# Performance work log

Measured on AMD Instinct MI355X. Metric: run time of the kernel, lower is better.

Reference implementation:

```python
import jax, jax.numpy as jnp
import numpy as np

N_NODES, N_EDGES, D, H = 100000, 640000, 128, 128


def setup_inputs() -> dict:
    key = jax.random.key(0)
    k = jax.random.split(key, 5)
    x = jax.random.normal(k[0], (N_NODES, D), dtype=jnp.float32)
    edge_idx = jax.random.randint(k[1], (2, N_EDGES), 0, N_NODES)
    eps = jnp.zeros((1,), dtype=jnp.float32)  # nn.Parameter(torch.zeros(1))
    # MLP params: Linear(D,H) -> ReLU -> Linear(H,D)
    W1 = jax.random.normal(k[2], (D, H), dtype=jnp.float32) / np.sqrt(D).astype(np.float32)
    b1 = jnp.zeros((H,), dtype=jnp.float32)
    W2 = jax.random.normal(k[3], (H, D), dtype=jnp.float32) / np.sqrt(H).astype(np.float32)
    b2 = jnp.zeros((D,), dtype=jnp.float32)
    return dict(x=x, edge_idx=edge_idx, eps=eps, W1=W1, b1=b1, W2=W2, b2=b2)


def reference(x, edge_idx, eps, W1, b1, W2, b2):
    # gather src node features, scatter-add into dst rows
    src, dst = edge_idx[0], edge_idx[1]
    agg = jax.ops.segment_sum(x[src], dst, num_segments=x.shape[0])  # [N, D]
    out = (1.0 + eps) * x + agg  # eps-weighted residual
    h = jax.nn.relu(out @ W1 + b1)
    return h @ W2 + b2
```

## Files before the change

### kernel.cpp

```cpp
#include <hip/hip_runtime.h>

#define DD 128
typedef unsigned int uint;
typedef unsigned short ushort;

typedef __attribute__((ext_vector_type(8))) __bf16 bf16x8;
typedef __attribute__((ext_vector_type(8))) short short8;
typedef __attribute__((ext_vector_type(4))) float f32x4;

__device__ inline short f2bf_bits(float f) {
  union { float f; unsigned u; } x; x.f = f;
  unsigned r = x.u + 0x7fffu + ((x.u >> 16) & 1u);
  return (short)(r >> 16);
}
__device__ inline float bflo(uint u) { return __uint_as_float(u << 16); }
__device__ inline float bfhi(uint u) { return __uint_as_float(u & 0xffff0000u); }

__global__ void k_zero(int* __restrict__ p, int n) {
  int i = blockIdx.x * blockDim.x + threadIdx.x;
  if (i < n) p[i] = 0;
}

#define CHUNK 2048
__global__ __launch_bounds__(256) void k_bin(const int* __restrict__ ei, int ne,
                                             int* __restrict__ scur, uint* __restrict__ pairs32,
                                             const float4* __restrict__ xf4,
                                             short8* __restrict__ xb8, int nx8,
                                             const float* __restrict__ W1,
                                             const float* __restrict__ W2,
                                             ushort* __restrict__ wbf, int nbins) {
  __shared__ uint st[CHUNK];
  __shared__ ushort stb[CHUNK];
  __shared__ int hist[512];
  __shared__ int sc[512];
  __shared__ int loff[512];
  __shared__ int cur[512];
  __shared__ int gb[512];

  const int tid = threadIdx.x;
  const int sb = blockIdx.x & 63;
  const long base = (long)blockIdx.x * CHUNK;
  int m = (int)(ne - base);
  if (m > CHUNK) m = CHUNK;
  if (m < 0) m = 0;

  const int i0 = tid, i1 = tid + 256;
  hist[i0] = 0; hist[i1] = 0;
  cur[i0] = 0;  cur[i1] = 0;
  __syncthreads();

  uint wreg[8];
  int breg[8];
#pragma unroll
  for (int i = 0; i < 8; ++i) {
    int idx = i * 256 + tid;
    if (idx < m) {
      uint s = (uint)ei[base + idx];
      uint d = (uint)ei[(long)ne + base + idx];
      breg[i] = (int)(d >> 8);
      wreg[i] = (s << 8) | (d & 255u);
      atomicAdd(&hist[breg[i]], 1);
    } else {
      breg[i] = -1;
    }
  }
  __syncthreads();

  sc[i0] = hist[i0]; sc[i1] = hist[i1];
  __syncthreads();
  for (int d = 1; d < 512; d <<= 1) {
    int t0 = (i0 >= d) ? sc[i0 - d] : 0;
    int t1 = (i1 >= d) ? sc[i1 - d] : 0;
    __syncthreads();
    sc[i0] += t0; sc[i1] += t1;
    __syncthreads();
  }
  loff[i0] = sc[i0] - hist[i0];
  loff[i1] = sc[i1] - hist[i1];
  if (i0 < nbins && hist[i0] > 0) gb[i0] = atomicAdd(&scur[i0 * 64 + sb], hist[i0]);
  if (i1 < nbins && hist[i1] > 0) gb[i1] = atomicAdd(&scur[i1 * 64 + sb], hist[i1]);
  __syncthreads();

#pragma unroll
  for (int i = 0; i < 8; ++i) {
    if (breg[i] >= 0) {
      int p = atomicAdd(&cur[breg[i]], 1);
      int pos = loff[breg[i]] + p;
      st[pos] = wreg[i];
      stb[pos] = (ushort)breg[i];
    }
  }
  __syncthreads();

  for (int i = tid; i < m; i += 256) {
    int b = stb[i];
    int k = i - loff[b];
    int g = gb[b] + k;
    if (g < 128)
      pairs32[(long)b * 16384 + (sb << 8) + g] = st[i];
  }

  int t = blockIdx.x * 256 + tid;
  int stride = gridDim.x * 256;
  for (int c = t; c < nx8; c += stride) {
    float4 a = xf4[2 * c], b = xf4[2 * c + 1];
    short8 o;
    o[0] = f2bf_bits(a.x); o[1] = f2bf_bits(a.y); o[2] = f2bf_bits(a.z); o[3] = f2bf_bits(a.w);
    o[4] = f2bf_bits(b.x); o[5] = f2bf_bits(b.y); o[6] = f2bf_bits(b.z); o[7] = f2bf_bits(b.w);
    xb8[c] = o;
  }
  if (t < 16384) {
    int k = t >> 7, n = t & 127;
    wbf[128 * n + 8 * ((k >> 3) ^ (n & 7)) + (k & 7)] = (ushort)f2bf_bits(W1[t]);
  } else if (t < 32768) {
    int e = t - 16384;
    int k = e >> 7, n = e & 127;
    wbf[16384 + 128 * n + 8 * ((k >> 3) ^ (n & 7)) + (k & 7)] = (ushort)f2bf_bits(W2[e]);
  }
}

#define SUBCAP 128
__global__ __launch_bounds__(256) void k_bucket(const uint* __restrict__ pairs32,
                                                const int* __restrict__ scur,
                                                int* __restrict__ slot,
                                                int* __restrict__ cnt, int n) {
  __shared__ uint st[64 * SUBCAP];
  __shared__ int cs[64];
  __shared__ int cur[256];
  const int b = blockIdx.x;
  const int tid = threadIdx.x;
  if (tid < 64) {
    int c = scur[b * 64 + tid];
    cs[tid] = c < SUBCAP ? c : SUBCAP;
  }
  cur[tid] = 0;
  __syncthreads();
  for (int k = tid; k < 64 * SUBCAP; k += 256) {
    int s = k >> 7, i = k & (SUBCAP - 1);
    if (i < cs[s]) st[k] = pairs32[(long)b * 16384 + (s << 8) + i];
  }
  __syncthreads();
  for (int k = tid; k < 64 * SUBCAP; k += 256) {
    int s = k >> 7, i = k & (SUBCAP - 1);
    if (i < cs[s]) {
      uint w = st[k];
      int d = (int)(w & 255u);
      int p = atomicAdd(&cur[d], 1);
      if (p < 64) slot[(long)b * 16384 + d * 64 + p] = (int)(w >> 8);
    }
  }
  __syncthreads();
  int node = (b << 8) + tid;
  if (node < n) cnt[node] = cur[tid];
}

__global__ __launch_bounds__(256) void k_agg4(const uint* __restrict__ xb,
                                              const float* __restrict__ eps,
                                              const int* __restrict__ cnt,
                                              const int* __restrict__ slot,
                                              uint* __restrict__ agb, int n) {
  int wv = (blockIdx.x * 256 + threadIdx.x) >> 6;
  int lane = threadIdx.x & 63;
  int r0 = wv * 4;
  if (r0 >= n) return;
  float s = 1.0f + eps[0];

  float ax[4], ay[4];
  int m[4], src[4];
  int mm = 0;
#pragma unroll
  for (int q = 0; q < 4; ++q) {
    int r = r0 + q;
    if (r < n) {
      uint u = xb[(long)r * 64 + lane];
      ax[q] = s * bflo(u); ay[q] = s * bfhi(u);
      int d = cnt[r];
      m[q] = d < 64 ? d : 64;
      src[q] = (lane < m[q]) ? slot[(long)r * 64 + lane] : 0;
      mm = m[q] > mm ? m[q] : mm;
    } else {
      ax[q] = 0.0f; ay[q] = 0.0f; m[q] = 0; src[q] = 0;
    }
  }

  for (int j = 0; j < mm; j += 4) {
    uint v[4][4];
#pragma unroll
    for (int q = 0; q < 4; ++q) {
#pragma unroll
      for (int k = 0; k < 4; ++k) {
        if (j + k < m[q]) {
          int ss = __shfl(src[q], j + k);
          v[q][k] = xb[(long)ss * 64 + lane];
        }
      }
    }
#pragma unroll
    for (int q = 0; q < 4; ++q) {
#pragma unroll
      for (int k = 0; k < 4; ++k) {
        if (j + k < m[q]) { ax[q] += bflo(v[q][k]); ay[q] += bfhi(v[q][k]); }
      }
    }
  }

#pragma unroll
  for (int q = 0; q < 4; ++q) {
    int r = r0 + q;
    if (r < n) {
      uint o = ((uint)(ushort)f2bf_bits(ay[q]) << 16) | (uint)(ushort)f2bf_bits(ax[q]);
      agb[(long)r * 64 + lane] = o;
    }
  }
}

__global__ __launch_bounds__(256) void k_mlp_bf(const ushort* __restrict__ agb,
                                                const ushort* __restrict__ wbf,
                                                const float* __restrict__ b1,
                                                const float* __restrict__ b2,
                                                float* __restrict__ out, int nrows) {
  __shared__ __align__(16) short Wt[2 * 16384];
  __shared__ __align__(16) short Hb[4][16 * 128];

  const int tid = threadIdx.x;
  const int lane = tid & 63;
  const int w = tid >> 6;
  const int l15 = lane & 15;
  const int g = lane >> 4;
  const int brow = blockIdx.x * 128;

  {
    const short8* ws8 = (const short8*)wbf;
    short8* wd8 = (short8*)Wt;
#pragma unroll
    for (int it = 0; it < 16; ++it) wd8[it * 256 + tid] = ws8[it * 256 + tid];
  }

  union U8 { short8 s; bf16x8 b; };

  U8 afr[2][4];
#pragma unroll
  for (int h = 0; h < 2; ++h) {
    int arow = brow + 64 * h + 16 * w + l15;
    if (arow < nrows) {
      const short8* ap = reinterpret_cast<const short8*>(agb + (long)arow * DD);
#pragma unroll
      for (int s = 0; s < 4; ++s) afr[h][s].s = ap[4 * s + g];
    } else {
#pragma unroll
      for (int s = 0; s < 4; ++s) {
        short8 t;
#pragma unroll
        for (int jj = 0; jj < 8; ++jj) t[jj] = 0;
        afr[h][s].s = t;
      }
    }
  }

  __syncthreads();

#pragma unroll
  for (int h = 0; h < 2; ++h) {
    const int wrow = brow + 64 * h + 16 * w;

    f32x4 acc[8];
#pragma unroll
    for (int nf = 0; nf < 8; ++nf) acc[nf] = (f32x4)(0.0f);
#pragma unroll
    for (int s = 0; s < 4; ++s) {
#pragma unroll
      for (int nf = 0; nf < 8; ++nf) {
        int n = 16 * nf + l15;
        U8 bf;
        bf.s = *reinterpret_cast<const short8*>(&Wt[128 * n + 8 * (((s << 2) | g) ^ (n & 7))]);
        acc[nf] = __builtin_amdgcn_mfma_f32_16x16x32_bf16(afr[h][s].b, bf.b, acc[nf], 0, 0, 0);
      }
    }

#pragma unroll
    for (int nf = 0; nf < 8; ++nf) {
      int col = 16 * nf + l15;
      float bb = b1[col];
#pragma unroll
      for (int i = 0; i < 4; ++i) {
        int hrow = 4 * g + i;
        float v = acc[nf][i] + bb;
        v = fmaxf(v, 0.0f);
        Hb[w][128 * hrow + 8 * ((col >> 3) ^ (hrow & 7)) + (col & 7)] = f2bf_bits(v);
      }
    }

    U8 hfr[4];
#pragma unroll
    for (int s = 0; s < 4; ++s) {
      hfr[s].s = *reinterpret_cast<const short8*>(
          &Hb[w][128 * l15 + 8 * (((s << 2) | g) ^ (l15 & 7))]);
    }

    f32x4 acc2[8];
#pragma unroll
    for (int nf = 0; nf < 8; ++nf) acc2[nf] = (f32x4)(0.0f);
#pragma unroll
    for (int s = 0; s < 4; ++s) {
#pragma unroll
      for (int nf = 0; nf < 8; ++nf) {
        int n = 16 * nf + l15;
        U8 bf;
        bf.s = *reinterpret_cast<const short8*>(
            &Wt[16384 + 128 * n + 8 * (((s << 2) | g) ^ (n & 7))]);
        acc2[nf] = __builtin_amdgcn_mfma_f32_16x16x32_bf16(hfr[s].b, bf.b, acc2[nf], 0, 0, 0);
      }
    }

#pragma unroll
    for (int nf = 0; nf < 8; ++nf) {
      int col = 16 * nf + l15;
      float bb = b2[col];
#pragma unroll
      for (int i = 0; i < 4; ++i) {
        int grow = wrow + 4 * g + i;
        if (grow < nrows) out[(long)grow * DD + col] = acc2[nf][i] + bb;
      }
    }
  }
}

extern "C" void kernel_launch(void* const* d_in, const int* in_sizes, int n_in,
                              void* d_out, int out_size, void* d_ws, size_t ws_size,
                              hipStream_t stream) {
  const float* x   = (const float*)d_in[0];
  const int*   ei  = (const int*)d_in[1];
  const float* eps = (const float*)d_in[2];
  const float* W1  = (const float*)d_in[3];
  const float* b1  = (const float*)d_in[4];
  const float* W2  = (const float*)d_in[5];
  const float* b2  = (const float*)d_in[6];
  float* out = (float*)d_out;

  const int N  = in_sizes[0] / DD;
  const int NE = in_sizes[1] / 2;
  const int NBINS = (N + 255) >> 8;

  ushort* wbf = (ushort*)d_ws;
  ushort* xbf = wbf + 32768;
  uint* region = (uint*)(xbf + (size_t)N * DD);
  int* slot = (int*)region;
  uint* agb = region;
  int* scur = (int*)(region + (size_t)NBINS * 16384);
  int* cnt = scur + (size_t)NBINS * 64;

  int nz = NBINS * 64;
  k_zero<<<(nz + 255) / 256, 256, 0, stream>>>(scur, nz);

  int nblk = (NE + CHUNK - 1) / CHUNK;
  k_bin<<<nblk, 256, 0, stream>>>(
      ei, NE, scur, region, (const float4*)x, (short8*)xbf, N * (DD / 8),
      W1, W2, wbf, NBINS);

  k_bucket<<<NBINS, 256, 0, stream>>>(region, scur, slot, cnt, N);

  int nwv = (N + 3) / 4;
  k_agg4<<<(nwv * 64 + 255) / 256, 256, 0, stream>>>(
      (const uint*)xbf, eps, cnt, slot, agb, N);

  k_mlp_bf<<<(N + 127) / 128, 256, 0, stream>>>(
      (const ushort*)agb, wbf, b1, b2, out, N);
}
```

Before: 117.8 us.

## Fuse neighbor aggregation with MLP kernel, staging aggregated rows in LDS

Result: slower. 259.2 us (+120.0%).

```diff
diff --git a/kernel.cpp b/kernel.cpp
--- a/kernel.cpp
+++ b/kernel.cpp
@@ -154,73 +154,16 @@
   if (node < n) cnt[node] = cur[tid];
 }
 
-__global__ __launch_bounds__(256) void k_agg4(const uint* __restrict__ xb,
-                                              const float* __restrict__ eps,
-                                              const int* __restrict__ cnt,
-                                              const int* __restrict__ slot,
-                                              uint* __restrict__ agb, int n) {
-  int wv = (blockIdx.x * 256 + threadIdx.x) >> 6;
-  int lane = threadIdx.x & 63;
-  int r0 = wv * 4;
-  if (r0 >= n) return;
-  float s = 1.0f + eps[0];
-
-  float ax[4], ay[4];
-  int m[4], src[4];
-  int mm = 0;
-#pragma unroll
-  for (int q = 0; q < 4; ++q) {
-    int r = r0 + q;
-    if (r < n) {
-      uint u = xb[(long)r * 64 + lane];
-      ax[q] = s * bflo(u); ay[q] = s * bfhi(u);
-      int d = cnt[r];
-      m[q] = d < 64 ? d : 64;
-      src[q] = (lane < m[q]) ? slot[(long)r * 64 + lane] : 0;
-      mm = m[q] > mm ? m[q] : mm;
-    } else {
-      ax[q] = 0.0f; ay[q] = 0.0f; m[q] = 0; src[q] = 0;
-    }
-  }
-
-  for (int j = 0; j < mm; j += 4) {
-    uint v[4][4];
-#pragma unroll
-    for (int q = 0; q < 4; ++q) {
-#pragma unroll
-      for (int k = 0; k < 4; ++k) {
-        if (j + k < m[q]) {
-          int ss = __shfl(src[q], j + k);
-          v[q][k] = xb[(long)ss * 64 + lane];
-        }
-      }
-    }
-#pragma unroll
-    for (int q = 0; q < 4; ++q) {
-#pragma unroll
-      for (int k = 0; k < 4; ++k) {
-        if (j + k < m[q]) { ax[q] += bflo(v[q][k]); ay[q] += bfhi(v[q][k]); }
-      }
-    }
-  }
-
-#pragma unroll
-  for (int q = 0; q < 4; ++q) {
-    int r = r0 + q;
-    if (r < n) {
-      uint o = ((uint)(ushort)f2bf_bits(ay[q]) << 16) | (uint)(ushort)f2bf_bits(ax[q]);
-      agb[(long)r * 64 + lane] = o;
-    }
-  }
-}
-
-__global__ __launch_bounds__(256) void k_mlp_bf(const ushort* __restrict__ agb,
-                                                const ushort* __restrict__ wbf,
-                                                const float* __restrict__ b1,
-                                                const float* __restrict__ b2,
-                                                float* __restrict__ out, int nrows) {
-  __shared__ __align__(16) short Wt[2 * 16384];
-  __shared__ __align__(16) short Hb[4][16 * 128];
+__global__ __launch_bounds__(256) void k_fused(const uint* __restrict__ xb,
+                                               const float* __restrict__ eps,
+                                               const int* __restrict__ cnt,
+                                               const int* __restrict__ slot,
+                                               const ushort* __restrict__ wbf,
+                                               const float* __restrict__ b1,
+                                               const float* __restrict__ b2,
+                                               float* __restrict__ out, int n) {
+  __shared__ __align__(16) short Wt[16384];
+  __shared__ __align__(16) short Ab[4][32 * 128];
 
   const int tid = threadIdx.x;
   const int lane = tid & 63;
@@ -228,55 +171,90 @@
   const int l15 = lane & 15;
   const int g = lane >> 4;
   const int brow = blockIdx.x * 128;
+  const int wrow0 = brow + 32 * w;
 
   {
     const short8* ws8 = (const short8*)wbf;
     short8* wd8 = (short8*)Wt;
 #pragma unroll
-    for (int it = 0; it < 16; ++it) wd8[it * 256 + tid] = ws8[it * 256 + tid];
-  }
-
-  union U8 { short8 s; bf16x8 b; };
-
-  U8 afr[2][4];
+    for (int it = 0; it < 8; ++it) wd8[it * 256 + tid] = ws8[it * 256 + tid];
+  }
+
+  float s = 1.0f + eps[0];
+  uint* abu = (uint*)&Ab[w][0];
+  for (int grp = 0; grp < 8; ++grp) {
+    int q0 = grp * 4;
+    float ax[4], ay[4];
+    int m[4], src[4];
+    int mm = 0;
+#pragma unroll
+    for (int q = 0; q < 4; ++q) {
+      int r = wrow0 + q0 + q;
+      if (r < n) {
+        uint u = xb[(long)r * 64 + lane];
+        ax[q] = s * bflo(u); ay[q] = s * bfhi(u);
+        int d = cnt[r];
+        m[q] = d < 64 ? d : 64;
+        src[q] = (lane < m[q]) ? slot[(long)r * 64 + lane] : 0;
+        mm = m[q] > mm ? m[q] : mm;
+      } else {
+        ax[q] = 0.0f; ay[q] = 0.0f; m[q] = 0; src[q] = 0;
+      }
+    }
+    for (int j = 0; j < mm; j += 4) {
+      uint v[4][4];
+#pragma unroll
+      for (int q = 0; q < 4; ++q) {
+#pragma unroll
+        for (int k = 0; k < 4; ++k) {
+          if (j + k < m[q]) {
+            int ss = __shfl(src[q], j + k);
+            v[q][k] = xb[(long)ss * 64 + lane];
+          }
+        }
+      }
+#pragma unroll
+      for (int q = 0; q < 4; ++q) {
+#pragma unroll
+        for (int k = 0; k < 4; ++k) {
+          if (j + k < m[q]) { ax[q] += bflo(v[q][k]); ay[q] += bfhi(v[q][k]); }
+        }
+      }
+    }
+#pragma unroll
+    for (int q = 0; q < 4; ++q) {
+      int rl = q0 + q;
+      uint o = ((uint)(ushort)f2bf_bits(ay[q]) << 16) | (uint)(ushort)f2bf_bits(ax[q]);
+      abu[rl * 64 + ((((lane >> 2) ^ (rl & 7)) << 2) | (lane & 3))] = o;
+    }
+  }
+
+  __syncthreads();
+
+  union U8 { short8 ss; bf16x8 b; };
+
 #pragma unroll
   for (int h = 0; h < 2; ++h) {
-    int arow = brow + 64 * h + 16 * w + l15;
-    if (arow < nrows) {
-      const short8* ap = reinterpret_cast<const short8*>(agb + (long)arow * DD);
-#pragma unroll
-      for (int s = 0; s < 4; ++s) afr[h][s].s = ap[4 * s + g];
-    } else {
-#pragma unroll
-      for (int s = 0; s < 4; ++s) {
-        short8 t;
-#pragma unroll
-        for (int jj = 0; jj < 8; ++jj) t[jj] = 0;
-        afr[h][s].s = t;
-      }
-    }
-  }
-
-  __syncthreads();
-
-#pragma unroll
-  for (int h = 0; h < 2; ++h) {
-    const int wrow = brow + 64 * h + 16 * w;
-
+    U8 afr[4];
+#pragma unroll
+    for (int s4 = 0; s4 < 4; ++s4) {
+      afr[s4].ss = *reinterpret_cast<const short8*>(
+          &Ab[w][(16 * h + l15) * 128 + (((4 * s4 + g) ^ (l15 & 7)) << 3)]);
+    }
     f32x4 acc[8];
 #pragma unroll
     for (int nf = 0; nf < 8; ++nf) acc[nf] = (f32x4)(0.0f);
 #pragma unroll
-    for (int s = 0; s < 4; ++s) {
+    for (int s4 = 0; s4 < 4; ++s4) {
 #pragma unroll
       for (int nf = 0; nf < 8; ++nf) {
-        int n = 16 * nf + l15;
+        int nn = 16 * nf + l15;
         U8 bf;
-        bf.s = *reinterpret_cast<const short8*>(&Wt[128 * n + 8 * (((s << 2) | g) ^ (n & 7))]);
-        acc[nf] = __builtin_amdgcn_mfma_f32_16x16x32_bf16(afr[h][s].b, bf.b, acc[nf], 0, 0, 0);
-      }
-    }
-
+        bf.ss = *reinterpret_cast<const short8*>(
+            &Wt[128 * nn + 8 * (((s4 << 2) | g) ^ (nn & 7))]);
+        acc[nf] = __builtin_amdgcn_mfma_f32_16x16x32_bf16(afr[s4].b, bf.b, acc[nf], 0, 0, 0);
+      }
+    }
 #pragma unroll
     for (int nf = 0; nf < 8; ++nf) {
       int col = 16 * nf + l15;
@@ -286,40 +264,50 @@
         int hrow = 4 * g + i;
         float v = acc[nf][i] + bb;
         v = fmaxf(v, 0.0f);
-        Hb[w][128 * hrow + 8 * ((col >> 3) ^ (hrow & 7)) + (col & 7)] = f2bf_bits(v);
-      }
-    }
-
+        Ab[w][(16 * h + hrow) * 128 + 8 * ((col >> 3) ^ (hrow & 7)) + (col & 7)] = f2bf_bits(v);
+      }
+    }
+  }
+
+  __syncthreads();
+  {
+    const short8* ws8 = (const short8*)(wbf + 16384);
+    short8* wd8 = (short8*)Wt;
+#pragma unroll
+    for (int it = 0; it < 8; ++it) wd8[it * 256 + tid] = ws8[it * 256 + tid];
+  }
+  __syncthreads();
+
+#pragma unroll
+  for (int h = 0; h < 2; ++h) {
     U8 hfr[4];
 #pragma unroll
-    for (int s = 0; s < 4; ++s) {
-      hfr[s].s = *reinterpret_cast<const short8*>(
-          &Hb[w][128 * l15 + 8 * (((s << 2) | g) ^ (l15 & 7))]);
-    }
-
+    for (int s4 = 0; s4 < 4; ++s4) {
+      hfr[s4].ss = *reinterpret_cast<const short8*>(
+          &Ab[w][(16 * h + l15) * 128 + 8 * (((s4 << 2) | g) ^ (l15 & 7))]);
+    }
     f32x4 acc2[8];
 #pragma unroll
     for (int nf = 0; nf < 8; ++nf) acc2[nf] = (f32x4)(0.0f);
 #pragma unroll
-    for (int s = 0; s < 4; ++s) {
+    for (int s4 = 0; s4 < 4; ++s4) {
 #pragma unroll
       for (int nf = 0; nf < 8; ++nf) {
-        int n = 16 * nf + l15;
+        int nn = 16 * nf + l15;
         U8 bf;
-        bf.s = *reinterpret_cast<const short8*>(
-            &Wt[16384 + 128 * n + 8 * (((s << 2) | g) ^ (n & 7))]);
-        acc2[nf] = __builtin_amdgcn_mfma_f32_16x16x32_bf16(hfr[s].b, bf.b, acc2[nf], 0, 0, 0);
-      }
-    }
-
+        bf.ss = *reinterpret_cast<const short8*>(
+            &Wt[128 * nn + 8 * (((s4 << 2) | g) ^ (nn & 7))]);
+        acc2[nf] = __builtin_amdgcn_mfma_f32_16x16x32_bf16(hfr[s4].b, bf.b, acc2[nf], 0, 0, 0);
+      }
+    }
 #pragma unroll
     for (int nf = 0; nf < 8; ++nf) {
       int col = 16 * nf + l15;
       float bb = b2[col];
 #pragma unroll
       for (int i = 0; i < 4; ++i) {
-        int grow = wrow + 4 * g + i;
-        if (grow < nrows) out[(long)grow * DD + col] = acc2[nf][i] + bb;
+        int grow = wrow0 + 16 * h + 4 * g + i;
+        if (grow < n) out[(long)grow * DD + col] = acc2[nf][i] + bb;
       }
     }
   }
@@ -345,7 +333,6 @@
   ushort* xbf = wbf + 32768;
   uint* region = (uint*)(xbf + (size_t)N * DD);
   int* slot = (int*)region;
-  uint* agb = region;
   int* scur = (int*)(region + (size_t)NBINS * 16384);
   int* cnt = scur + (size_t)NBINS * 64;
 
@@ -359,10 +346,6 @@
 
   k_bucket<<<NBINS, 256, 0, stream>>>(region, scur, slot, cnt, N);
 
-  int nwv = (N + 3) / 4;
-  k_agg4<<<(nwv * 64 + 255) / 256, 256, 0, stream>>>(
-      (const uint*)xbf, eps, cnt, slot, agb, N);
-
-  k_mlp_bf<<<(N + 127) / 128, 256, 0, stream>>>(
-      (const ushort*)agb, wbf, b1, b2, out, N);
-}
+  k_fused<<<(N + 127) / 128, 256, 0, stream>>>(
+      (const uint*)xbf, eps, cnt, slot, wbf, b1, b2, out, N);
+}
```
